# Optimization experiments

Hardware: AMD Instinct MI355X
Metric: run time of the kernel (lower is better)

Reference implementation:

```python
import jax, jax.numpy as jnp
import numpy as np

OBS, H, F1, A, T, B = 128, 128, 256, 18, 128, 1024


def _ln(x, w, b, eps=1e-5):
    mu = jnp.mean(x, -1, keepdims=True)
    xc = x - mu
    var = jnp.mean(xc * xc, -1, keepdims=True)
    return xc * jax.lax.rsqrt(var + eps) * w + b


def _features(x, w1, b1, w2, b2, lnw, lnb):
    h = jax.nn.relu(x @ w1.T + b1)      # [N, 256]
    h = h @ w2.T + b2                   # [N, 128]
    return jax.nn.relu(_ln(h, lnw, lnb))


def _masked_lstm(xs, ds, h0, c0, wih, whh, b):
    # xs: [T,B,H], ds: [T,B] float; PyTorch gate order i,f,g,o
    def step(carry, inp):
        h, c = carry
        xt, dt = inp
        m = (1.0 - dt)[:, None]
        h = h * m
        c = c * m
        g = xt @ wih.T + h @ whh.T + b  # [B, 4H]
        i, f, gg, o = jnp.split(g, 4, axis=-1)
        c = jax.nn.sigmoid(f) * c + jax.nn.sigmoid(i) * jnp.tanh(gg)
        h = jax.nn.sigmoid(o) * jnp.tanh(c)
        return (h, c), h
    (hT, cT), hs = jax.lax.scan(step, (h0, c0), (xs, ds))
    return hs, hT, cT


def setup_inputs() -> dict:
    key = jax.random.key(0)
    ks = iter(jax.random.split(key, 64))
    p = lambda shape, s=0.05: jax.random.normal(next(ks), shape, jnp.float32) * s
    inp = {
        'x': jax.random.normal(next(ks), (T * B, OBS), jnp.float32),
        'actor_h': jnp.zeros((1, B, H), jnp.float32),
        'actor_c': jnp.zeros((1, B, H), jnp.float32),
        'critic_h': jnp.zeros((1, B, H), jnp.float32),
        'critic_c': jnp.zeros((1, B, H), jnp.float32),
        'done': jax.random.randint(next(ks), (T * B,), 0, 2, jnp.int32),
        'action': jax.random.randint(next(ks), (T * B,), 0, A, jnp.int64),
        # actor params
        'af_w1': p((F1, OBS)), 'af_b1': p((F1,)),
        'af_w2': p((H, F1)), 'af_b2': p((H,)),
        'af_lnw': jnp.ones((H,), jnp.float32), 'af_lnb': jnp.zeros((H,), jnp.float32),
        'a_wih': p((4 * H, H)), 'a_whh': p((4 * H, H)), 'a_b': p((4 * H,)),
        'a_lnw': jnp.ones((H,), jnp.float32), 'a_lnb': jnp.zeros((H,), jnp.float32),
        'a_hw': p((A, H)), 'a_hb': p((A,)),
        # critic params
        'cf_w1': p((F1, OBS)), 'cf_b1': p((F1,)),
        'cf_w2': p((H, F1)), 'cf_b2': p((H,)),
        'cf_lnw': jnp.ones((H,), jnp.float32), 'cf_lnb': jnp.zeros((H,), jnp.float32),
        'c_wih': p((4 * H, H)), 'c_whh': p((4 * H, H)), 'c_b': p((4 * H,)),
        'c_lnw': jnp.ones((H,), jnp.float32), 'c_lnb': jnp.zeros((H,), jnp.float32),
        'c_hw': p((1, H)), 'c_hb': p((1,)),
    }
    return inp


def reference(x, actor_h, actor_c, critic_h, critic_c,
              af_w1, af_b1, af_w2, af_b2, af_lnw, af_lnb,
              a_wih, a_whh, a_b, a_lnw, a_lnb, a_hw, a_hb,
              cf_w1, cf_b1, cf_w2, cf_b2, cf_lnw, cf_lnb,
              c_wih, c_whh, c_b, c_lnw, c_lnb, c_hw, c_hb,
              done, action):
    bsz = actor_h.shape[1]
    ds = done.astype(jnp.float32).reshape(-1, bsz)  # [T, B]

    # actor branch
    af = _features(x, af_w1, af_b1, af_w2, af_b2, af_lnw, af_lnb).reshape(-1, bsz, H)
    hs, ahT, acT = _masked_lstm(af, ds, actor_h[0], actor_c[0], a_wih, a_whh, a_b)
    ah = _ln(hs.reshape(-1, H), a_lnw, a_lnb)
    logits = ah @ a_hw.T + a_hb                     # [N, A]
    logp_all = jax.nn.log_softmax(logits)
    logp = jnp.take_along_axis(logp_all, action[:, None], axis=1)[:, 0]
    entropy = -jnp.sum(jnp.exp(logp_all) * logp_all, axis=-1)

    # critic branch
    cf = _features(x, cf_w1, cf_b1, cf_w2, cf_b2, cf_lnw, cf_lnb).reshape(-1, bsz, H)
    cs, chT, ccT = _masked_lstm(cf, ds, critic_h[0], critic_c[0], c_wih, c_whh, c_b)
    ch = _ln(cs.reshape(-1, H), c_lnw, c_lnb)
    value = ch @ c_hw.T + c_hb                      # [N, 1]

    return (action, logp, entropy, value,
            ahT[None], acT[None], chT[None], ccT[None])
```

## Files before the change

kernel.cpp:

```cpp
#include <hip/hip_runtime.h>
#include <stdint.h>
#include <stddef.h>

#define OBS 128
#define F1D 256
#define HD  128
#define NA  18
#define TT  128
#define BB  1024
#define NN  (TT*BB)
#define LOG2E 1.442695041f

typedef __attribute__((ext_vector_type(8))) short short8;
typedef __attribute__((ext_vector_type(4))) float f32x4;

__device__ __forceinline__ unsigned short f2bf(float f) {
  union { float f; uint32_t u; } v; v.f = f;
  uint32_t u = v.u;
  u += 0x7fffu + ((u >> 16) & 1u);
  return (unsigned short)(u >> 16);
}
__device__ __forceinline__ float bf2f(uint32_t hu) {
  union { uint32_t u; float f; } v; v.u = hu << 16;
  return v.f;
}
__device__ __forceinline__ f32x4 mfma16(short8 a, short8 b, f32x4 c) {
  return __builtin_amdgcn_mfma_f32_16x16x32_bf16(a, b, c, 0, 0, 0);
}
__device__ __forceinline__ short8 cvt8(const float* p, float sc) {
  float4 a = *(const float4*)p;
  float4 b = *(const float4*)(p + 4);
  union { unsigned short u[8]; short8 s; } o;
  o.u[0]=f2bf(a.x*sc); o.u[1]=f2bf(a.y*sc); o.u[2]=f2bf(a.z*sc); o.u[3]=f2bf(a.w*sc);
  o.u[4]=f2bf(b.x*sc); o.u[5]=f2bf(b.y*sc); o.u[6]=f2bf(b.z*sc); o.u[7]=f2bf(b.w*sc);
  return o.s;
}
__device__ __forceinline__ short8 pin(short8 v) {
  int4 i = *(int4*)&v;
  asm volatile("" : "+v"(i.x), "+v"(i.y), "+v"(i.z), "+v"(i.w));
  return *(short8*)&i;
}

__global__ __launch_bounds__(512, 2) void fused_kernel(
    const float* __restrict__ x, const int* __restrict__ done,
    const int* __restrict__ action,
    const float* __restrict__ aw1, const float* __restrict__ ab1,
    const float* __restrict__ aw2, const float* __restrict__ ab2,
    const float* __restrict__ aflnw, const float* __restrict__ aflnb,
    const float* __restrict__ awih, const float* __restrict__ awhh,
    const float* __restrict__ a_b,
    const float* __restrict__ alnw, const float* __restrict__ alnb,
    const float* __restrict__ ahw, const float* __restrict__ ahb,
    const float* __restrict__ cw1, const float* __restrict__ cb1,
    const float* __restrict__ cw2, const float* __restrict__ cb2,
    const float* __restrict__ cflnw, const float* __restrict__ cflnb,
    const float* __restrict__ cwih, const float* __restrict__ cwhh,
    const float* __restrict__ c_b,
    const float* __restrict__ clnw, const float* __restrict__ clnb,
    const float* __restrict__ chw, const float* __restrict__ chb,
    const float* __restrict__ ah0, const float* __restrict__ ac0,
    const float* __restrict__ ch0, const float* __restrict__ cc0,
    unsigned short* __restrict__ featg, float* __restrict__ dout)
{
  int g = blockIdx.x;
  int br = g >> 7;
  int chunk = g & 127;
  int base8 = chunk * 8;

  const float* w1  = br ? cw1 : aw1;
  const float* b1  = br ? cb1 : ab1;
  const float* w2  = br ? cw2 : aw2;
  const float* b2  = br ? cb2 : ab2;
  const float* flw = br ? cflnw : aflnw;
  const float* flb = br ? cflnb : aflnb;
  const float* wih = br ? cwih : awih;
  const float* whh = br ? cwhh : awhh;
  const float* gb  = br ? c_b : a_b;
  const float* h0  = br ? ch0 : ah0;
  const float* c0  = br ? cc0 : ac0;
  unsigned short* feat = featg + (size_t)br * NN * HD;

  __shared__ __align__(16) char smemA[51200];
  __shared__ float mls[(TT+1)*8];
  __shared__ unsigned short hlds[2][8*128];
  __shared__ float pa[HD], pb[HD], cws[HD];
  __shared__ float hbl[NA];
  __shared__ float cbsS;
  __shared__ int flagS;

  int tid = threadIdx.x;
  int w = tid >> 6, lane = tid & 63, q = lane >> 4, ln = lane & 15;
  int team = tid >> 8, t_tid = tid & 255, w4 = w & 3;

  {
    unsigned short* xst  = (unsigned short*)smemA + team*4096;
    unsigned short* h1st = (unsigned short*)(smemA + 16384) + team*8192;
    float*          lnst = (float*)(smemA + 49152) + team*256;

    short8 b1f[4][4]; float b1v[4];
    #pragma unroll
    for (int ct = 0; ct < 4; ++ct) {
      int nn = w4*64 + ct*16 + ln;
      b1v[ct] = b1[nn];
      #pragma unroll
      for (int kf = 0; kf < 4; ++kf)
        b1f[ct][kf] = pin(cvt8(&w1[nn*OBS + kf*32 + q*8], 1.0f));
    }
    short8 b2f[2][8]; float b2v[2], lwv[2], lbv[2];
    #pragma unroll
    for (int nt = 0; nt < 2; ++nt) {
      int nn = w4*32 + nt*16 + ln;
      b2v[nt] = b2[nn]; lwv[nt] = flw[nn]; lbv[nt] = flb[nn];
      #pragma unroll
      for (int kf = 0; kf < 8; ++kf)
        b2f[nt][kf] = pin(cvt8(&w2[nn*F1D + kf*32 + q*8], 1.0f));
    }
    float4 xr[4];
    #pragma unroll
    for (int s = 0; s < 4; ++s) {
      int e4 = t_tid + s*256;
      int r = e4 >> 5, c4 = e4 & 31;
      size_t grow = (size_t)(team*4 + (r>>3))*BB + base8 + (r&7);
      xr[s] = ((const float4*)x)[grow*32 + c4];
    }
    for (int j = 0; j < 16; ++j) {
      int jj = j*2 + team;
      #pragma unroll
      for (int s = 0; s < 4; ++s) {
        int e = (t_tid + s*256) * 4;
        int r = e >> 7, k = e & 127;
        int ad = r*128 + ((((k>>3) ^ (r&15)) << 3)) + (k&7);
        uint2 d;
        d.x = (uint32_t)f2bf(xr[s].x) | ((uint32_t)f2bf(xr[s].y) << 16);
        d.y = (uint32_t)f2bf(xr[s].z) | ((uint32_t)f2bf(xr[s].w) << 16);
        *(uint2*)&xst[ad] = d;
      }
      __syncthreads();
      {
        int jjn = (j < 15) ? jj + 2 : jj;
        #pragma unroll
        for (int s = 0; s < 4; ++s) {
          int e4 = t_tid + s*256;
          int r = e4 >> 5, c4 = e4 & 31;
          size_t grow = (size_t)(jjn*4 + (r>>3))*BB + base8 + (r&7);
          xr[s] = ((const float4*)x)[grow*32 + c4];
        }
      }
      short8 af[2][4];
      #pragma unroll
      for (int mt = 0; mt < 2; ++mt)
        #pragma unroll
        for (int kf = 0; kf < 4; ++kf)
          af[mt][kf] = *(const short8*)&xst[(mt*16 + ln)*128 + ((((kf<<2)|q) ^ ln) << 3)];
      #pragma unroll
      for (int ct = 0; ct < 4; ++ct) {
        int nn = w4*64 + ct*16 + ln;
        #pragma unroll
        for (int mt = 0; mt < 2; ++mt) {
          f32x4 acc = {b1v[ct], b1v[ct], b1v[ct], b1v[ct]};
          #pragma unroll
          for (int kf = 0; kf < 4; ++kf) acc = mfma16(af[mt][kf], b1f[ct][kf], acc);
          #pragma unroll
          for (int rg = 0; rg < 4; ++rg) {
            float v = acc[rg] > 0.0f ? acc[rg] : 0.0f;
            int rrow = mt*16 + q*4 + rg;
            h1st[rrow*256 + (((nn>>3) ^ (rrow&15)) << 3) + (nn&7)] = f2bf(v);
          }
        }
      }
      __syncthreads();
      f32x4 acc2[2][2];
      #pragma unroll
      for (int mt = 0; mt < 2; ++mt) {
        short8 ah[8];
        #pragma unroll
        for (int kf = 0; kf < 8; ++kf)
          ah[kf] = *(const short8*)&h1st[(mt*16 + ln)*256 + ((((kf<<2)|q) ^ ln) << 3)];
        #pragma unroll
        for (int nt = 0; nt < 2; ++nt) {
          f32x4 acc = {b2v[nt], b2v[nt], b2v[nt], b2v[nt]};
          #pragma unroll
          for (int kf = 0; kf < 8; ++kf) acc = mfma16(ah[kf], b2f[nt][kf], acc);
          acc2[nt][mt] = acc;
        }
      }
      #pragma unroll
      for (int mt = 0; mt < 2; ++mt)
        #pragma unroll
        for (int rg = 0; rg < 4; ++rg) {
          float s = acc2[0][mt][rg] + acc2[1][mt][rg];
          float ssq = acc2[0][mt][rg]*acc2[0][mt][rg] + acc2[1][mt][rg]*acc2[1][mt][rg];
          #pragma unroll
          for (int m = 1; m < 16; m <<= 1) { s += __shfl_xor(s, m); ssq += __shfl_xor(ssq, m); }
          if (ln == 0) {
            int r = mt*16 + q*4 + rg;
            lnst[r*8 + w4*2]     = s;
            lnst[r*8 + w4*2 + 1] = ssq;
          }
        }
      __syncthreads();
      #pragma unroll
      for (int mt = 0; mt < 2; ++mt)
        #pragma unroll
        for (int rg = 0; rg < 4; ++rg) {
          int r = mt*16 + q*4 + rg;
          float4 p0 = *(const float4*)&lnst[r*8];
          float4 p1 = *(const float4*)&lnst[r*8 + 4];
          float S  = p0.x + p0.z + p1.x + p1.z;
          float SS = p0.y + p0.w + p1.y + p1.w;
          float mu = S * (1.0f/128.0f);
          float var = SS * (1.0f/128.0f) - mu*mu;
          float rstd = rsqrtf(var + 1e-5f);
          size_t grow = (size_t)(jj*4 + (r>>3))*BB + base8 + (r&7);
          #pragma unroll
          for (int nt = 0; nt < 2; ++nt) {
            float t = (acc2[nt][mt][rg] - mu) * rstd * lwv[nt] + lbv[nt];
            if (t < 0.0f) t = 0.0f;
            feat[grow*HD + w4*32 + nt*16 + ln] = f2bf(t);
          }
        }
      __syncthreads();
    }
  }

  int n = w*16 + ln;
  {
    short8 bfr[4][8]; float bias[4];
    #pragma unroll
    for (int g4 = 0; g4 < 4; ++g4) {
      int gn = g4*128 + n;
      float sc = (g4 == 2) ? -2.0f*LOG2E : -LOG2E;
      bias[g4] = gb[gn] * sc;
      #pragma unroll
      for (int kf = 0; kf < 8; ++kf) {
        const float* src = (kf < 4) ? &wih[gn*HD + kf*32 + q*8]
                                    : &whh[gn*HD + (kf-4)*32 + q*8];
        bfr[g4][kf] = pin(cvt8(src, sc));
      }
    }
    for (int i = tid; i < (TT+1)*8; i += 512)
      mls[i] = (i < TT*8) ? 1.0f - (float)done[(i>>3)*BB + base8 + (i&7)] : 1.0f;

    const int loff = (base8 + (ln>>1))*HD + q*8;
    int soff[2], hoffw[2], haddr[4];
    #pragma unroll
    for (int j = 0; j < 2; ++j) {
      int r = q*2 + j;
      soff[j]  = (base8 + r)*HD + n;
      hoffw[j] = r*128 + (((n>>3) ^ r) << 3) + (n&7);
    }
    #pragma unroll
    for (int kf = 0; kf < 4; ++kf) {
      int rr = ln >> 1;
      haddr[kf] = rr*128 + ((((kf<<2)|q) ^ rr) << 3);
    }
    float hp[2], cp[2]; unsigned short hu_prev[2];
    #pragma unroll
    for (int j = 0; j < 2; ++j) {
      int b = base8 + q*2 + j;
      hp[j] = h0[b*HD + n];
      cp[j] = c0[b*HD + n];
      hu_prev[j] = 0;
    }
    short8 afr[4], nfr[4];
    #pragma unroll
    for (int kf = 0; kf < 4; ++kf)
      afr[kf] = *(const short8*)&feat[loff + kf*32];
    __syncthreads();
    #pragma unroll
    for (int j = 0; j < 2; ++j) {
      float m = mls[q*2 + j];
      cp[j] *= m;
      hlds[0][hoffw[j]] = f2bf(hp[j] * m);
    }
    __syncthreads();

#define LSTM_STEP(TTT, CUR, NXT, HB)                                           \
  {                                                                            \
    short8 hfr[4];                                                             \
    _Pragma("unroll")                                                          \
    for (int kf = 0; kf < 4; ++kf)                                             \
      hfr[kf] = *(const short8*)&hlds[HB][haddr[kf]];                          \
    {                                                                          \
      int tp = (TTT) > 0 ? (TTT) - 1 : 0;                                      \
      unsigned short* sq = feat + (size_t)tp * (BB*HD);                        \
      sq[soff[0]] = hu_prev[0];                                                \
      sq[soff[1]] = hu_prev[1];                                                \
    }                                                                          \
    int tn = ((TTT) + 1 < TT) ? (TTT) + 1 : TT - 1;                            \
    const unsigned short* fq = feat + (size_t)tn * (BB*HD);                    \
    _Pragma("unroll")                                                          \
    for (int kf = 0; kf < 4; ++kf)                                             \
      NXT[kf] = *(const short8*)&fq[loff + kf*32];                             \
    f32x4 a0 = {bias[0],bias[0],bias[0],bias[0]};                              \
    f32x4 a1 = {bias[1],bias[1],bias[1],bias[1]};                              \
    f32x4 a2 = {bias[2],bias[2],bias[2],bias[2]};                              \
    f32x4 a3 = {bias[3],bias[3],bias[3],bias[3]};                              \
    _Pragma("unroll")                                                          \
    for (int kf = 0; kf < 4; ++kf) {                                           \
      a0 = mfma16(CUR[kf], bfr[0][kf], a0);                                    \
      a1 = mfma16(CUR[kf], bfr[1][kf], a1);                                    \
      a2 = mfma16(CUR[kf], bfr[2][kf], a2);                                    \
      a3 = mfma16(CUR[kf], bfr[3][kf], a3);                                    \
    }                                                                          \
    _Pragma("unroll")                                                          \
    for (int kf = 0; kf < 4; ++kf) {                                           \
      a0 = mfma16(hfr[kf], bfr[0][4+kf], a0);                                  \
      a1 = mfma16(hfr[kf], bfr[1][4+kf], a1);                                  \
      a2 = mfma16(hfr[kf], bfr[2][4+kf], a2);                                  \
      a3 = mfma16(hfr[kf], bfr[3][4+kf], a3);                                  \
    }                                                                          \
    float2 mn = *(const float2*)&mls[((TTT)+1)*8 + q*2];                       \
    _Pragma("unroll")                                                          \
    for (int j = 0; j < 2; ++j) {                                              \
      int rg = j*2;     \
      float si = __builtin_amdgcn_rcpf(1.0f + __builtin_amdgcn_exp2f(a0[rg])); \
      float sf = __builtin_amdgcn_rcpf(1.0f + __builtin_amdgcn_exp2f(a1[rg])); \
      float tg = __builtin_fmaf(2.0f,                                          \
                   __builtin_amdgcn_rcpf(1.0f + __builtin_amdgcn_exp2f(a2[rg])), -1.0f); \
      float so = __builtin_amdgcn_rcpf(1.0f + __builtin_amdgcn_exp2f(a3[rg])); \
      float cn = __builtin_fmaf(sf, cp[j], si*tg);                             \
      float th = __builtin_fmaf(2.0f,                                          \
                   __builtin_amdgcn_rcpf(1.0f + __builtin_amdgcn_exp2f(-2.0f*LOG2E*cn)), -1.0f); \
      float hn = so * th;                                                      \
      unsigned short hu = f2bf(hn);                                            \
      hu_prev[j] = hu;                                                         \
      bool live = ((&mn.x)[j] != 0.0f);                                        \
      cp[j] = live ? cn : 0.0f;                                                \
      hp[j] = hn;                                                              \
      hlds[(HB)^1][hoffw[j]] = live ? hu : (unsigned short)0;                  \
    }                                                                          \
    __syncthreads();                                                           \
  }

    for (int t = 0; t < TT; t += 2) {
      LSTM_STEP(t,   afr, nfr, 0)
      LSTM_STEP(t+1, nfr, afr, 1)
    }
#undef LSTM_STEP

    {
      unsigned short* sq = feat + (size_t)(TT-1)*(BB*HD);
      sq[soff[0]] = hu_prev[0];
      sq[soff[1]] = hu_prev[1];
    }
    {
      float* outh = dout + (size_t)(4 + br*2) * NN;
      float* outc = dout + (size_t)(5 + br*2) * NN;
      #pragma unroll
      for (int j = 0; j < 2; ++j) {
        int b = base8 + q*2 + j;
        outh[b*HD + n] = hp[j];
        outc[b*HD + n] = cp[j];
      }
    }
  }

  if (tid == 0) flagS = 0;
  if (tid < HD) {
    pa[tid] = br ? clnw[tid] : alnw[tid];
    pb[tid] = br ? clnb[tid] : alnb[tid];
    if (br) cws[tid] = chw[tid];
  }
  int localf = 0;
  if (br == 0) {
    if (tid < NA) hbl[tid] = ahb[tid];
    for (int i = 2*tid + 1; i < 4096; i += 1024) localf |= action[i];
  } else if (tid == 0) cbsS = chb[0];
  __syncthreads();
  if (localf) flagS = 1;
  __syncthreads();

  int sub = tid & 3, kidx = tid >> 2;
  if (br == 0) {
    unsigned short* hsn = (unsigned short*)smemA;
    float* co = (float*)(smemA + 32768);
    short8 hbf[2][4];
    #pragma unroll
    for (int nt = 0; nt < 2; ++nt) {
      int nn = nt*16 + ln;
      #pragma unroll
      for (int kf = 0; kf < 4; ++kf) {
        short8 z = {0,0,0,0,0,0,0,0};
        hbf[nt][kf] = (nn < NA) ? pin(cvt8(&ahw[nn*HD + kf*32 + q*8], 1.0f)) : z;
      }
    }
    int fl = flagS;
    for (int ch = 0; ch < 8; ++ch) {
      {
        int k = ch*128 + kidx;
        int rrow = (k >> 3)*BB + base8 + (k & 7);
        const unsigned short* hp2 = feat + (size_t)rrow*HD + sub*32;
        uint4 d0 = *(const uint4*)hp2;
        uint4 d1 = *(const uint4*)(hp2 + 8);
        uint4 d2 = *(const uint4*)(hp2 + 16);
        uint4 d3 = *(const uint4*)(hp2 + 24);
        float nv[32];
        #define UP(W_, B_) { nv[B_] = bf2f((W_) & 0xffffu); nv[(B_)+1] = bf2f((W_) >> 16); }
        UP(d0.x,0) UP(d0.y,2) UP(d0.z,4) UP(d0.w,6)
        UP(d1.x,8) UP(d1.y,10) UP(d1.z,12) UP(d1.w,14)
        UP(d2.x,16) UP(d2.y,18) UP(d2.z,20) UP(d2.w,22)
        UP(d3.x,24) UP(d3.y,26) UP(d3.z,28) UP(d3.w,30)
        #undef UP
        float s = 0.0f, ssq = 0.0f;
        #pragma unroll
        for (int j = 0; j < 32; ++j) { s += nv[j]; ssq += nv[j]*nv[j]; }
        s += __shfl_xor(s, 1); ssq += __shfl_xor(ssq, 1);
        s += __shfl_xor(s, 2); ssq += __shfl_xor(ssq, 2);
        float mu = s * (1.0f/128.0f);
        float var = ssq * (1.0f/128.0f) - mu*mu;
        float rstd = rsqrtf(var + 1e-5f);
        #pragma unroll
        for (int cc = 0; cc < 4; ++cc) {
          unsigned short ob[8];
          #pragma unroll
          for (int j = 0; j < 8; ++j) {
            int c = sub*32 + cc*8 + j;
            ob[j] = f2bf((nv[cc*8+j] - mu) * rstd * pa[c] + pb[c]);
          }
          int c8 = sub*4 + cc;
          *(short8*)&hsn[kidx*128 + ((c8 ^ (kidx & 15)) << 3)] = *(short8*)ob;
        }
      }
      __syncthreads();
      {
        short8 afh[4];
        #pragma unroll
        for (int kf = 0; kf < 4; ++kf)
          afh[kf] = *(const short8*)&hsn[(w*16 + ln)*128 + ((((kf<<2)|q) ^ ln) << 3)];
        #pragma unroll
        for (int nt = 0; nt < 2; ++nt) {
          f32x4 acc = {0.0f, 0.0f, 0.0f, 0.0f};
          #pragma unroll
          for (int kf = 0; kf < 4; ++kf) acc = mfma16(afh[kf], hbf[nt][kf], acc);
          #pragma unroll
          for (int rg = 0; rg < 4; ++rg)
            co[(w*16 + q*4 + rg)*36 + nt*16 + ln] = acc[rg];
        }
      }
      __syncthreads();
      if (tid < 128) {
        int k = ch*128 + tid;
        int rrow = (k >> 3)*BB + base8 + (k & 7);
        int act = fl ? action[rrow] : (int)(((const long long*)action)[rrow]);
        dout[rrow] = (float)act;
        int aidx = act < 0 ? 0 : (act > NA-1 ? NA-1 : act);
        float lg[NA];
        #pragma unroll
        for (int a = 0; a < NA; ++a) lg[a] = co[tid*36 + a] + hbl[a];
        float mx = lg[0];
        #pragma unroll
        for (int a = 1; a < NA; ++a) mx = fmaxf(mx, lg[a]);
        float se = 0.0f;
        #pragma unroll
        for (int a = 0; a < NA; ++a) se += __expf(lg[a] - mx);
        float lse = __logf(se);
        float lpa = 0.0f, ent = 0.0f;
        #pragma unroll
        for (int a = 0; a < NA; ++a) {
          float lp = lg[a] - mx - lse;
          ent -= __expf(lp) * lp;
          lpa += (a == aidx) ? lp : 0.0f;
        }
        dout[(size_t)NN + rrow] = lpa;
        dout[(size_t)2*NN + rrow] = ent;
      }
      __syncthreads();
    }
  } else {
    for (int ch = 0; ch < 8; ++ch) {
      int k = ch*128 + kidx;
      int rrow = (k >> 3)*BB + base8 + (k & 7);
      const unsigned short* hp2 = feat + (size_t)rrow*HD + sub*32;
      uint4 d0 = *(const uint4*)hp2;
      uint4 d1 = *(const uint4*)(hp2 + 8);
      uint4 d2 = *(const uint4*)(hp2 + 16);
      uint4 d3 = *(const uint4*)(hp2 + 24);
      float nv[32];
      #define UP(W_, B_) { nv[B_] = bf2f((W_) & 0xffffu); nv[(B_)+1] = bf2f((W_) >> 16); }
      UP(d0.x,0) UP(d0.y,2) UP(d0.z,4) UP(d0.w,6)
      UP(d1.x,8) UP(d1.y,10) UP(d1.z,12) UP(d1.w,14)
      UP(d2.x,16) UP(d2.y,18) UP(d2.z,20) UP(d2.w,22)
      UP(d3.x,24) UP(d3.y,26) UP(d3.z,28) UP(d3.w,30)
      #undef UP
      float s = 0.0f, ssq = 0.0f;
      #pragma unroll
      for (int j = 0; j < 32; ++j) { s += nv[j]; ssq += nv[j]*nv[j]; }
      s += __shfl_xor(s, 1); ssq += __shfl_xor(ssq, 1);
      s += __shfl_xor(s, 2); ssq += __shfl_xor(ssq, 2);
      float mu = s * (1.0f/128.0f);
      float var = ssq * (1.0f/128.0f) - mu*mu;
      float rstd = rsqrtf(var + 1e-5f);
      float dot = 0.0f;
      #pragma unroll
      for (int j = 0; j < 32; ++j) {
        int c = sub*32 + j;
        dot += ((nv[j] - mu) * rstd * pa[c] + pb[c]) * cws[c];
      }
      dot += __shfl_xor(dot, 1);
      dot += __shfl_xor(dot, 2);
      if (sub == 0) dout[(size_t)3*NN + rrow] = dot + cbsS;
    }
  }
}

extern "C" void kernel_launch(void* const* d_in, const int* in_sizes, int n_in,
                              void* d_out, int out_size, void* d_ws, size_t ws_size,
                              hipStream_t stream) {
  (void)in_sizes; (void)n_in; (void)out_size; (void)ws_size;
  const float* x    = (const float*)d_in[0];
  const float* ah0  = (const float*)d_in[1];
  const float* ac0  = (const float*)d_in[2];
  const float* ch0  = (const float*)d_in[3];
  const float* cc0  = (const float*)d_in[4];
  const int*   done = (const int*)d_in[5];
  const int*   act  = (const int*)d_in[6];
  const float* aw1  = (const float*)d_in[7];
  const float* ab1  = (const float*)d_in[8];
  const float* aw2  = (const float*)d_in[9];
  const float* ab2  = (const float*)d_in[10];
  const float* aflnw= (const float*)d_in[11];
  const float* aflnb= (const float*)d_in[12];
  const float* awih = (const float*)d_in[13];
  const float* awhh = (const float*)d_in[14];
  const float* a_b  = (const float*)d_in[15];
  const float* alnw = (const float*)d_in[16];
  const float* alnb = (const float*)d_in[17];
  const float* ahw  = (const float*)d_in[18];
  const float* ahb  = (const float*)d_in[19];
  const float* cw1  = (const float*)d_in[20];
  const float* cb1  = (const float*)d_in[21];
  const float* cw2  = (const float*)d_in[22];
  const float* cb2  = (const float*)d_in[23];
  const float* cflnw= (const float*)d_in[24];
  const float* cflnb= (const float*)d_in[25];
  const float* cwih = (const float*)d_in[26];
  const float* cwhh = (const float*)d_in[27];
  const float* c_b  = (const float*)d_in[28];
  const float* clnw = (const float*)d_in[29];
  const float* clnb = (const float*)d_in[30];
  const float* chw  = (const float*)d_in[31];
  const float* chb  = (const float*)d_in[32];

  unsigned short* featb = (unsigned short*)d_ws;
  float* out = (float*)d_out;

  fused_kernel<<<256, 512, 0, stream>>>(
      x, done, act,
      aw1, ab1, aw2, ab2, aflnw, aflnb, awih, awhh, a_b, alnw, alnb, ahw, ahb,
      cw1, cb1, cw2, cb2, cflnw, cflnb, cwih, cwhh, c_b, clnw, clnb, chw, chb,
      ah0, ac0, ch0, cc0,
      featb, out);
}
```

Baseline: 413.3 us.

## Split feature MLP and LSTM into separate kernels, use packed bf16 conversion

Splits the single fused kernel into a feature-MLP kernel and an LSTM/head kernel so each has a smaller register and LDS footprint. Replaces software round-to-nearest bf16 conversion with the hardware v_cvt_pk_bf16_f32 instruction throughout. Reorders the mask and store logic in the LSTM step to pack two outputs per conversion. This adds a kernel launch and gives up any overlap between feature computation and the recurrence inside one block.

Result: slower. 434.9 us (+5.2%).

```diff
diff --git a/kernel.cpp b/kernel.cpp
--- a/kernel.cpp
+++ b/kernel.cpp
@@ -24,15 +24,22 @@
   union { uint32_t u; float f; } v; v.u = hu << 16;
   return v.f;
 }
+__device__ __forceinline__ uint32_t pk2(float lo, float hi) {
+  uint32_t r;
+  asm("v_cvt_pk_bf16_f32 %0, %1, %2" : "=v"(r) : "v"(lo), "v"(hi));
+  return r;
+}
 __device__ __forceinline__ f32x4 mfma16(short8 a, short8 b, f32x4 c) {
   return __builtin_amdgcn_mfma_f32_16x16x32_bf16(a, b, c, 0, 0, 0);
 }
 __device__ __forceinline__ short8 cvt8(const float* p, float sc) {
   float4 a = *(const float4*)p;
   float4 b = *(const float4*)(p + 4);
-  union { unsigned short u[8]; short8 s; } o;
-  o.u[0]=f2bf(a.x*sc); o.u[1]=f2bf(a.y*sc); o.u[2]=f2bf(a.z*sc); o.u[3]=f2bf(a.w*sc);
-  o.u[4]=f2bf(b.x*sc); o.u[5]=f2bf(b.y*sc); o.u[6]=f2bf(b.z*sc); o.u[7]=f2bf(b.w*sc);
+  union { uint32_t u[4]; short8 s; } o;
+  o.u[0] = pk2(a.x*sc, a.y*sc);
+  o.u[1] = pk2(a.z*sc, a.w*sc);
+  o.u[2] = pk2(b.x*sc, b.y*sc);
+  o.u[3] = pk2(b.z*sc, b.w*sc);
   return o.s;
 }
 __device__ __forceinline__ short8 pin(short8 v) {
@@ -41,19 +48,177 @@
   return *(short8*)&i;
 }
 
-__global__ __launch_bounds__(512, 2) void fused_kernel(
-    const float* __restrict__ x, const int* __restrict__ done,
-    const int* __restrict__ action,
+__global__ __launch_bounds__(512, 2) void feat_kernel(
+    const float* __restrict__ x,
     const float* __restrict__ aw1, const float* __restrict__ ab1,
     const float* __restrict__ aw2, const float* __restrict__ ab2,
     const float* __restrict__ aflnw, const float* __restrict__ aflnb,
+    const float* __restrict__ cw1, const float* __restrict__ cb1,
+    const float* __restrict__ cw2, const float* __restrict__ cb2,
+    const float* __restrict__ cflnw, const float* __restrict__ cflnb,
+    unsigned short* __restrict__ featg)
+{
+  int g = blockIdx.x;
+  int br = g >> 7;
+  int chunk = g & 127;
+  int base8 = chunk * 8;
+
+  const float* w1  = br ? cw1 : aw1;
+  const float* b1  = br ? cb1 : ab1;
+  const float* w2  = br ? cw2 : aw2;
+  const float* b2  = br ? cb2 : ab2;
+  const float* flw = br ? cflnw : aflnw;
+  const float* flb = br ? cflnb : aflnb;
+  unsigned short* feat = featg + (size_t)br * NN * HD;
+
+  __shared__ __align__(16) char smemA[51200];
+
+  int tid = threadIdx.x;
+  int w = tid >> 6, lane = tid & 63, q = lane >> 4, ln = lane & 15;
+  int team = tid >> 8, t_tid = tid & 255, w4 = w & 3;
+
+  unsigned short* xst  = (unsigned short*)smemA + team*4096;
+  unsigned short* h1st = (unsigned short*)(smemA + 16384) + team*8192;
+  float*          lnst = (float*)(smemA + 49152) + team*256;
+
+  short8 b1f[4][4]; float b1v[4];
+  #pragma unroll
+  for (int ct = 0; ct < 4; ++ct) {
+    int nn = w4*64 + ct*16 + ln;
+    b1v[ct] = b1[nn];
+    #pragma unroll
+    for (int kf = 0; kf < 4; ++kf)
+      b1f[ct][kf] = pin(cvt8(&w1[nn*OBS + kf*32 + q*8], 1.0f));
+  }
+  short8 b2f[2][8]; float b2v[2], lwv[2], lbv[2];
+  #pragma unroll
+  for (int nt = 0; nt < 2; ++nt) {
+    int nn = w4*32 + nt*16 + ln;
+    b2v[nt] = b2[nn]; lwv[nt] = flw[nn]; lbv[nt] = flb[nn];
+    #pragma unroll
+    for (int kf = 0; kf < 8; ++kf)
+      b2f[nt][kf] = pin(cvt8(&w2[nn*F1D + kf*32 + q*8], 1.0f));
+  }
+  float4 xr[4];
+  #pragma unroll
+  for (int s = 0; s < 4; ++s) {
+    int e4 = t_tid + s*256;
+    int r = e4 >> 5, c4 = e4 & 31;
+    size_t grow = (size_t)(team*4 + (r>>3))*BB + base8 + (r&7);
+    xr[s] = ((const float4*)x)[grow*32 + c4];
+  }
+  for (int j = 0; j < 16; ++j) {
+    int jj = j*2 + team;
+    #pragma unroll
+    for (int s = 0; s < 4; ++s) {
+      int e = (t_tid + s*256) * 4;
+      int r = e >> 7, k = e & 127;
+      int ad = r*128 + ((((k>>3) ^ (r&15)) << 3)) + (k&7);
+      uint2 d;
+      d.x = pk2(xr[s].x, xr[s].y);
+      d.y = pk2(xr[s].z, xr[s].w);
+      *(uint2*)&xst[ad] = d;
+    }
+    __syncthreads();
+    {
+      int jjn = (j < 15) ? jj + 2 : jj;
+      #pragma unroll
+      for (int s = 0; s < 4; ++s) {
+        int e4 = t_tid + s*256;
+        int r = e4 >> 5, c4 = e4 & 31;
+        size_t grow = (size_t)(jjn*4 + (r>>3))*BB + base8 + (r&7);
+        xr[s] = ((const float4*)x)[grow*32 + c4];
+      }
+    }
+    short8 af[2][4];
+    #pragma unroll
+    for (int mt = 0; mt < 2; ++mt)
+      #pragma unroll
+      for (int kf = 0; kf < 4; ++kf)
+        af[mt][kf] = *(const short8*)&xst[(mt*16 + ln)*128 + ((((kf<<2)|q) ^ ln) << 3)];
+    #pragma unroll
+    for (int ct = 0; ct < 4; ++ct) {
+      int nn = w4*64 + ct*16 + ln;
+      #pragma unroll
+      for (int mt = 0; mt < 2; ++mt) {
+        f32x4 acc = {b1v[ct], b1v[ct], b1v[ct], b1v[ct]};
+        #pragma unroll
+        for (int kf = 0; kf < 4; ++kf) acc = mfma16(af[mt][kf], b1f[ct][kf], acc);
+        float v0 = acc[0] > 0.0f ? acc[0] : 0.0f;
+        float v1 = acc[1] > 0.0f ? acc[1] : 0.0f;
+        float v2 = acc[2] > 0.0f ? acc[2] : 0.0f;
+        float v3 = acc[3] > 0.0f ? acc[3] : 0.0f;
+        uint32_t p01 = pk2(v0, v1), p23 = pk2(v2, v3);
+        int r0 = mt*16 + q*4;
+        h1st[(r0+0)*256 + (((nn>>3) ^ ((r0+0)&15)) << 3) + (nn&7)] = (unsigned short)p01;
+        h1st[(r0+1)*256 + (((nn>>3) ^ ((r0+1)&15)) << 3) + (nn&7)] = (unsigned short)(p01 >> 16);
+        h1st[(r0+2)*256 + (((nn>>3) ^ ((r0+2)&15)) << 3) + (nn&7)] = (unsigned short)p23;
+        h1st[(r0+3)*256 + (((nn>>3) ^ ((r0+3)&15)) << 3) + (nn&7)] = (unsigned short)(p23 >> 16);
+      }
+    }
+    __syncthreads();
+    f32x4 acc2[2][2];
+    #pragma unroll
+    for (int mt = 0; mt < 2; ++mt) {
+      short8 ah[8];
+      #pragma unroll
+      for (int kf = 0; kf < 8; ++kf)
+        ah[kf] = *(const short8*)&h1st[(mt*16 + ln)*256 + ((((kf<<2)|q) ^ ln) << 3)];
+      #pragma unroll
+      for (int nt = 0; nt < 2; ++nt) {
+        f32x4 acc = {b2v[nt], b2v[nt], b2v[nt], b2v[nt]};
+        #pragma unroll
+        for (int kf = 0; kf < 8; ++kf) acc = mfma16(ah[kf], b2f[nt][kf], acc);
+        acc2[nt][mt] = acc;
+      }
+    }
+    #pragma unroll
+    for (int mt = 0; mt < 2; ++mt)
+      #pragma unroll
+      for (int rg = 0; rg < 4; ++rg) {
+        float s = acc2[0][mt][rg] + acc2[1][mt][rg];
+        float ssq = acc2[0][mt][rg]*acc2[0][mt][rg] + acc2[1][mt][rg]*acc2[1][mt][rg];
+        #pragma unroll
+        for (int m = 1; m < 16; m <<= 1) { s += __shfl_xor(s, m); ssq += __shfl_xor(ssq, m); }
+        if (ln == 0) {
+          int r = mt*16 + q*4 + rg;
+          lnst[r*8 + w4*2]     = s;
+          lnst[r*8 + w4*2 + 1] = ssq;
+        }
+      }
+    __syncthreads();
+    #pragma unroll
+    for (int mt = 0; mt < 2; ++mt)
+      #pragma unroll
+      for (int rg = 0; rg < 4; ++rg) {
+        int r = mt*16 + q*4 + rg;
+        float4 p0 = *(const float4*)&lnst[r*8];
+        float4 p1 = *(const float4*)&lnst[r*8 + 4];
+        float S  = p0.x + p0.z + p1.x + p1.z;
+        float SS = p0.y + p0.w + p1.y + p1.w;
+        float mu = S * (1.0f/128.0f);
+        float var = SS * (1.0f/128.0f) - mu*mu;
+        float rstd = rsqrtf(var + 1e-5f);
+        size_t grow = (size_t)(jj*4 + (r>>3))*BB + base8 + (r&7);
+        float t0 = (acc2[0][mt][rg] - mu) * rstd * lwv[0] + lbv[0];
+        float t1 = (acc2[1][mt][rg] - mu) * rstd * lwv[1] + lbv[1];
+        if (t0 < 0.0f) t0 = 0.0f;
+        if (t1 < 0.0f) t1 = 0.0f;
+        uint32_t p = pk2(t0, t1);
+        unsigned short* fp = &feat[grow*HD + w4*32 + ln];
+        fp[0]  = (unsigned short)p;
+        fp[16] = (unsigned short)(p >> 16);
+      }
+    __syncthreads();
+  }
+}
+
+__global__ __launch_bounds__(512, 2) void lstm_head_kernel(
+    const int* __restrict__ done, const int* __restrict__ action,
     const float* __restrict__ awih, const float* __restrict__ awhh,
     const float* __restrict__ a_b,
     const float* __restrict__ alnw, const float* __restrict__ alnb,
     const float* __restrict__ ahw, const float* __restrict__ ahb,
-    const float* __restrict__ cw1, const float* __restrict__ cb1,
-    const float* __restrict__ cw2, const float* __restrict__ cb2,
-    const float* __restrict__ cflnw, const float* __restrict__ cflnb,
     const float* __restrict__ cwih, const float* __restrict__ cwhh,
     const float* __restrict__ c_b,
     const float* __restrict__ clnw, const float* __restrict__ clnb,
@@ -67,12 +232,6 @@
   int chunk = g & 127;
   int base8 = chunk * 8;
 
-  const float* w1  = br ? cw1 : aw1;
-  const float* b1  = br ? cb1 : ab1;
-  const float* w2  = br ? cw2 : aw2;
-  const float* b2  = br ? cb2 : ab2;
-  const float* flw = br ? cflnw : aflnw;
-  const float* flb = br ? cflnb : aflnb;
   const float* wih = br ? cwih : awih;
   const float* whh = br ? cwhh : awhh;
   const float* gb  = br ? c_b : a_b;
@@ -80,7 +239,7 @@
   const float* c0  = br ? cc0 : ac0;
   unsigned short* feat = featg + (size_t)br * NN * HD;
 
-  __shared__ __align__(16) char smemA[51200];
+  __shared__ __align__(16) char smemC[51200];
   __shared__ float mls[(TT+1)*8];
   __shared__ unsigned short hlds[2][8*128];
   __shared__ float pa[HD], pb[HD], cws[HD];
@@ -90,138 +249,6 @@
 
   int tid = threadIdx.x;
   int w = tid >> 6, lane = tid & 63, q = lane >> 4, ln = lane & 15;
-  int team = tid >> 8, t_tid = tid & 255, w4 = w & 3;
-
-  {
-    unsigned short* xst  = (unsigned short*)smemA + team*4096;
-    unsigned short* h1st = (unsigned short*)(smemA + 16384) + team*8192;
-    float*          lnst = (float*)(smemA + 49152) + team*256;
-
-    short8 b1f[4][4]; float b1v[4];
-    #pragma unroll
-    for (int ct = 0; ct < 4; ++ct) {
-      int nn = w4*64 + ct*16 + ln;
-      b1v[ct] = b1[nn];
-      #pragma unroll
-      for (int kf = 0; kf < 4; ++kf)
-        b1f[ct][kf] = pin(cvt8(&w1[nn*OBS + kf*32 + q*8], 1.0f));
-    }
-    short8 b2f[2][8]; float b2v[2], lwv[2], lbv[2];
-    #pragma unroll
-    for (int nt = 0; nt < 2; ++nt) {
-      int nn = w4*32 + nt*16 + ln;
-      b2v[nt] = b2[nn]; lwv[nt] = flw[nn]; lbv[nt] = flb[nn];
-      #pragma unroll
-      for (int kf = 0; kf < 8; ++kf)
-        b2f[nt][kf] = pin(cvt8(&w2[nn*F1D + kf*32 + q*8], 1.0f));
-    }
-    float4 xr[4];
-    #pragma unroll
-    for (int s = 0; s < 4; ++s) {
-      int e4 = t_tid + s*256;
-      int r = e4 >> 5, c4 = e4 & 31;
-      size_t grow = (size_t)(team*4 + (r>>3))*BB + base8 + (r&7);
-      xr[s] = ((const float4*)x)[grow*32 + c4];
-    }
-    for (int j = 0; j < 16; ++j) {
-      int jj = j*2 + team;
-      #pragma unroll
-      for (int s = 0; s < 4; ++s) {
-        int e = (t_tid + s*256) * 4;
-        int r = e >> 7, k = e & 127;
-        int ad = r*128 + ((((k>>3) ^ (r&15)) << 3)) + (k&7);
-        uint2 d;
-        d.x = (uint32_t)f2bf(xr[s].x) | ((uint32_t)f2bf(xr[s].y) << 16);
-        d.y = (uint32_t)f2bf(xr[s].z) | ((uint32_t)f2bf(xr[s].w) << 16);
-        *(uint2*)&xst[ad] = d;
-      }
-      __syncthreads();
-      {
-        int jjn = (j < 15) ? jj + 2 : jj;
-        #pragma unroll
-        for (int s = 0; s < 4; ++s) {
-          int e4 = t_tid + s*256;
-          int r = e4 >> 5, c4 = e4 & 31;
-          size_t grow = (size_t)(jjn*4 + (r>>3))*BB + base8 + (r&7);
-          xr[s] = ((const float4*)x)[grow*32 + c4];
-        }
-      }
-      short8 af[2][4];
-      #pragma unroll
-      for (int mt = 0; mt < 2; ++mt)
-        #pragma unroll
-        for (int kf = 0; kf < 4; ++kf)
-          af[mt][kf] = *(const short8*)&xst[(mt*16 + ln)*128 + ((((kf<<2)|q) ^ ln) << 3)];
-      #pragma unroll
-      for (int ct = 0; ct < 4; ++ct) {
-        int nn = w4*64 + ct*16 + ln;
-        #pragma unroll
-        for (int mt = 0; mt < 2; ++mt) {
-          f32x4 acc = {b1v[ct], b1v[ct], b1v[ct], b1v[ct]};
-          #pragma unroll
-          for (int kf = 0; kf < 4; ++kf) acc = mfma16(af[mt][kf], b1f[ct][kf], acc);
-          #pragma unroll
-          for (int rg = 0; rg < 4; ++rg) {
-            float v = acc[rg] > 0.0f ? acc[rg] : 0.0f;
-            int rrow = mt*16 + q*4 + rg;
-            h1st[rrow*256 + (((nn>>3) ^ (rrow&15)) << 3) + (nn&7)] = f2bf(v);
-          }
-        }
-      }
-      __syncthreads();
-      f32x4 acc2[2][2];
-      #pragma unroll
-      for (int mt = 0; mt < 2; ++mt) {
-        short8 ah[8];
-        #pragma unroll
-        for (int kf = 0; kf < 8; ++kf)
-          ah[kf] = *(const short8*)&h1st[(mt*16 + ln)*256 + ((((kf<<2)|q) ^ ln) << 3)];
-        #pragma unroll
-        for (int nt = 0; nt < 2; ++nt) {
-          f32x4 acc = {b2v[nt], b2v[nt], b2v[nt], b2v[nt]};
-          #pragma unroll
-          for (int kf = 0; kf < 8; ++kf) acc = mfma16(ah[kf], b2f[nt][kf], acc);
-          acc2[nt][mt] = acc;
-        }
-      }
-      #pragma unroll
-      for (int mt = 0; mt < 2; ++mt)
-        #pragma unroll
-        for (int rg = 0; rg < 4; ++rg) {
-          float s = acc2[0][mt][rg] + acc2[1][mt][rg];
-          float ssq = acc2[0][mt][rg]*acc2[0][mt][rg] + acc2[1][mt][rg]*acc2[1][mt][rg];
-          #pragma unroll
-          for (int m = 1; m < 16; m <<= 1) { s += __shfl_xor(s, m); ssq += __shfl_xor(ssq, m); }
-          if (ln == 0) {
-            int r = mt*16 + q*4 + rg;
-            lnst[r*8 + w4*2]     = s;
-            lnst[r*8 + w4*2 + 1] = ssq;
-          }
-        }
-      __syncthreads();
-      #pragma unroll
-      for (int mt = 0; mt < 2; ++mt)
-        #pragma unroll
-        for (int rg = 0; rg < 4; ++rg) {
-          int r = mt*16 + q*4 + rg;
-          float4 p0 = *(const float4*)&lnst[r*8];
-          float4 p1 = *(const float4*)&lnst[r*8 + 4];
-          float S  = p0.x + p0.z + p1.x + p1.z;
-          float SS = p0.y + p0.w + p1.y + p1.w;
-          float mu = S * (1.0f/128.0f);
-          float var = SS * (1.0f/128.0f) - mu*mu;
-          float rstd = rsqrtf(var + 1e-5f);
-          size_t grow = (size_t)(jj*4 + (r>>3))*BB + base8 + (r&7);
-          #pragma unroll
-          for (int nt = 0; nt < 2; ++nt) {
-            float t = (acc2[nt][mt][rg] - mu) * rstd * lwv[nt] + lbv[nt];
-            if (t < 0.0f) t = 0.0f;
-            feat[grow*HD + w4*32 + nt*16 + ln] = f2bf(t);
-          }
-        }
-      __syncthreads();
-    }
-  }
 
   int n = w*16 + ln;
   {
@@ -262,16 +289,17 @@
       cp[j] = c0[b*HD + n];
       hu_prev[j] = 0;
     }
+    __syncthreads();
     short8 afr[4], nfr[4];
     #pragma unroll
     for (int kf = 0; kf < 4; ++kf)
       afr[kf] = *(const short8*)&feat[loff + kf*32];
-    __syncthreads();
-    #pragma unroll
-    for (int j = 0; j < 2; ++j) {
-      float m = mls[q*2 + j];
-      cp[j] *= m;
-      hlds[0][hoffw[j]] = f2bf(hp[j] * m);
+    {
+      float m0 = mls[q*2], m1 = mls[q*2 + 1];
+      cp[0] *= m0; cp[1] *= m1;
+      uint32_t hpk = pk2(hp[0]*m0, hp[1]*m1);
+      hlds[0][hoffw[0]] = (unsigned short)hpk;
+      hlds[0][hoffw[1]] = (unsigned short)(hpk >> 16);
     }
     __syncthreads();
 
@@ -310,7 +338,7 @@
       a2 = mfma16(hfr[kf], bfr[2][4+kf], a2);                                  \
       a3 = mfma16(hfr[kf], bfr[3][4+kf], a3);                                  \
     }                                                                          \
-    float2 mn = *(const float2*)&mls[((TTT)+1)*8 + q*2];                       \
+    float hnv[2], cnv[2];                                                      \
     _Pragma("unroll")                                                          \
     for (int j = 0; j < 2; ++j) {                                              \
       int rg = j*2;     \
@@ -322,14 +350,19 @@
       float cn = __builtin_fmaf(sf, cp[j], si*tg);                             \
       float th = __builtin_fmaf(2.0f,                                          \
                    __builtin_amdgcn_rcpf(1.0f + __builtin_amdgcn_exp2f(-2.0f*LOG2E*cn)), -1.0f); \
-      float hn = so * th;                                                      \
-      unsigned short hu = f2bf(hn);                                            \
-      hu_prev[j] = hu;                                                         \
-      bool live = ((&mn.x)[j] != 0.0f);                                        \
-      cp[j] = live ? cn : 0.0f;                                                \
-      hp[j] = hn;                                                              \
-      hlds[(HB)^1][hoffw[j]] = live ? hu : (unsigned short)0;                  \
+      hnv[j] = so * th;                                                        \
+      cnv[j] = cn;                                                             \
     }                                                                          \
+    uint32_t hpk = pk2(hnv[0], hnv[1]);                                        \
+    unsigned short hu0 = (unsigned short)hpk;                                  \
+    unsigned short hu1 = (unsigned short)(hpk >> 16);                          \
+    hu_prev[0] = hu0; hu_prev[1] = hu1;                                        \
+    float2 mn = *(const float2*)&mls[((TTT)+1)*8 + q*2];                       \
+    bool l0 = (mn.x != 0.0f), l1 = (mn.y != 0.0f);                             \
+    cp[0] = l0 ? cnv[0] : 0.0f; hp[0] = hnv[0];                                \
+    cp[1] = l1 ? cnv[1] : 0.0f; hp[1] = hnv[1];                                \
+    hlds[(HB)^1][hoffw[0]] = l0 ? hu0 : (unsigned short)0;                     \
+    hlds[(HB)^1][hoffw[1]] = l1 ? hu1 : (unsigned short)0;                     \
     __syncthreads();                                                           \
   }
 
@@ -373,8 +406,8 @@
 
   int sub = tid & 3, kidx = tid >> 2;
   if (br == 0) {
-    unsigned short* hsn = (unsigned short*)smemA;
-    float* co = (float*)(smemA + 32768);
+    unsigned short* hsn = (unsigned short*)smemC;
+    float* co = (float*)(smemC + 32768);
     short8 hbf[2][4];
     #pragma unroll
     for (int nt = 0; nt < 2; ++nt) {
@@ -412,14 +445,17 @@
         float rstd = rsqrtf(var + 1e-5f);
         #pragma unroll
         for (int cc = 0; cc < 4; ++cc) {
-          unsigned short ob[8];
+          float ov[8];
           #pragma unroll
           for (int j = 0; j < 8; ++j) {
             int c = sub*32 + cc*8 + j;
-            ob[j] = f2bf((nv[cc*8+j] - mu) * rstd * pa[c] + pb[c]);
+            ov[j] = (nv[cc*8+j] - mu) * rstd * pa[c] + pb[c];
           }
+          uint4 P;
+          P.x = pk2(ov[0], ov[1]); P.y = pk2(ov[2], ov[3]);
+          P.z = pk2(ov[4], ov[5]); P.w = pk2(ov[6], ov[7]);
           int c8 = sub*4 + cc;
-          *(short8*)&hsn[kidx*128 + ((c8 ^ (kidx & 15)) << 3)] = *(short8*)ob;
+          *(uint4*)&hsn[kidx*128 + ((c8 ^ (kidx & 15)) << 3)] = P;
         }
       }
       __syncthreads();
@@ -545,10 +581,14 @@
   unsigned short* featb = (unsigned short*)d_ws;
   float* out = (float*)d_out;
 
-  fused_kernel<<<256, 512, 0, stream>>>(
-      x, done, act,
-      aw1, ab1, aw2, ab2, aflnw, aflnb, awih, awhh, a_b, alnw, alnb, ahw, ahb,
-      cw1, cb1, cw2, cb2, cflnw, cflnb, cwih, cwhh, c_b, clnw, clnb, chw, chb,
+  feat_kernel<<<256, 512, 0, stream>>>(
+      x, aw1, ab1, aw2, ab2, aflnw, aflnb,
+      cw1, cb1, cw2, cb2, cflnw, cflnb, featb);
+
+  lstm_head_kernel<<<256, 512, 0, stream>>>(
+      done, act,
+      awih, awhh, a_b, alnw, alnb, ahw, ahb,
+      cwih, cwhh, c_b, clnw, clnb, chw, chb,
       ah0, ac0, ch0, cc0,
       featb, out);
 }
```
